# Kernel tuning notes

Measured on AMD Instinct MI355X. Metric: run time of the kernel, lower is better.

Reference implementation:

```python
import jax, jax.numpy as jnp
import numpy as np

D_MODEL = 1024
NUM_HEADS = 16
D_K = D_MODEL // NUM_HEADS
LN_EPS = 1e-5


def setup_inputs() -> dict:
    key = jax.random.key(0)
    ks = jax.random.split(key, 10)
    s = 1.0 / np.sqrt(D_MODEL)
    x = jax.random.normal(ks[0], (4, 2048, D_MODEL), dtype=jnp.float32)
    Wq = jax.random.uniform(ks[1], (D_MODEL, D_MODEL), jnp.float32, -s, s)
    bq = jax.random.uniform(ks[2], (D_MODEL,), jnp.float32, -s, s)
    Wk = jax.random.uniform(ks[3], (D_MODEL, D_MODEL), jnp.float32, -s, s)
    bk = jax.random.uniform(ks[4], (D_MODEL,), jnp.float32, -s, s)
    Wv = jax.random.uniform(ks[5], (D_MODEL, D_MODEL), jnp.float32, -s, s)
    bv = jax.random.uniform(ks[6], (D_MODEL,), jnp.float32, -s, s)
    Wo = jax.random.uniform(ks[7], (D_MODEL, D_MODEL), jnp.float32, -s, s)
    bo = jax.random.uniform(ks[8], (D_MODEL,), jnp.float32, -s, s)
    gamma = jnp.ones((D_MODEL,), jnp.float32)
    beta = jnp.zeros((D_MODEL,), jnp.float32)
    return {"x": x, "Wq": Wq, "bq": bq, "Wk": Wk, "bk": bk, "Wv": Wv,
            "bv": bv, "Wo": Wo, "bo": bo, "gamma": gamma, "beta": beta}


def reference(x, Wq, bq, Wk, bk, Wv, bv, Wo, bo, gamma, beta):
    B, S, D = x.shape
    H, dk = NUM_HEADS, D_K
    # torch Linear: y = x @ W.T + b
    def proj(W, b):
        y = jnp.einsum('bsd,ed->bse', x, W) + b
        return y.reshape(B, S, H, dk).transpose(0, 2, 1, 3)  # [B,H,S,dk]
    Q = proj(Wq, bq)
    K = proj(Wk, bk)
    V = proj(Wv, bv)
    scores = jnp.einsum('bhqd,bhkd->bhqk', Q, K) / np.sqrt(dk)
    attn = jax.nn.softmax(scores, axis=-1)
    head = jnp.einsum('bhqk,bhkd->bhqd', attn, V)
    head = head.transpose(0, 2, 1, 3).reshape(B, S, D)
    out = jnp.einsum('bsd,ed->bse', head, Wo) + bo
    # LayerNorm
    mu = jnp.mean(out, axis=-1, keepdims=True)
    var = jnp.var(out, axis=-1, keepdims=True)
    out = (out - mu) * jax.lax.rsqrt(var + LN_EPS) * gamma + beta
    # dropout is identity in eval mode
    return x + out
```

## Files before the change

### kernel.cpp

```cpp
#include <hip/hip_runtime.h>
#include <stdint.h>

typedef unsigned short u16;
typedef unsigned int u32;
typedef __attribute__((ext_vector_type(8))) short short8;
typedef __attribute__((ext_vector_type(4))) float f32x4;
typedef __attribute__((ext_vector_type(16))) float f32x16;
typedef __attribute__((ext_vector_type(4))) unsigned short u16x4;

#define DEV static __device__ __forceinline__

DEV float bf2f(u16 b) { return __uint_as_float(((uint32_t)b) << 16); }
DEV u16 f2bf(float f) {
  uint32_t u = __float_as_uint(f);
  u += 0x7FFFu + ((u >> 16) & 1u);
  return (u16)(u >> 16);
}
DEV void gld16(const u16* gsrc, u16* ldsdst) {
  __builtin_amdgcn_global_load_lds((const __attribute__((address_space(1))) void*)gsrc,
                                   (__attribute__((address_space(3))) void*)ldsdst, 16, 0, 0);
}
#define MFMA16(a, b, c) __builtin_amdgcn_mfma_f32_16x16x32_bf16(a, b, c, 0, 0, 0)
#define MFMA32(a, b, c) __builtin_amdgcn_mfma_f32_32x32x16_bf16(a, b, c, 0, 0, 0)

#define WAITVM4() asm volatile("s_waitcnt vmcnt(4)" ::: "memory")
#define WAITVM0() asm volatile("s_waitcnt vmcnt(0)" ::: "memory")
DEV void barrier() {
  asm volatile("" ::: "memory");
  __builtin_amdgcn_s_barrier();
  asm volatile("" ::: "memory");
}

#if __has_builtin(__builtin_amdgcn_exp2f)
DEV float fexp2(float x) { return __builtin_amdgcn_exp2f(x); }
#else
DEV float fexp2(float x) { return exp2f(x); }
#endif

DEV u32 cvtpk(float lo, float hi) {
  u32 r;
  asm("v_cvt_pk_bf16_f32 %0, %1, %2" : "=v"(r) : "v"(lo), "v"(hi));
  return r;
}

__global__ __launch_bounds__(256) void k_convert(
    const float* __restrict__ x, const float* __restrict__ wq, const float* __restrict__ wk,
    const float* __restrict__ wv, const float* __restrict__ wo, u16* __restrict__ ws)
{
  int bid = blockIdx.x, t = threadIdx.x;
  const float* src; u16* dst; size_t off;
  if (bid < 8192) { src = x; dst = ws; off = (size_t)bid * 1024; }
  else {
    int r = bid - 8192; int sel = r >> 10; int lb = r & 1023;
    src = sel == 0 ? wq : sel == 1 ? wk : sel == 2 ? wv : wo;
    dst = ws + 8388608u + (size_t)sel * 1048576u;
    off = (size_t)lb * 1024;
  }
  size_t e = off + (size_t)t * 4;
  f32x4 v = *(const f32x4*)(src + e);
  u16x4 o;
  o.x = f2bf(v.x); o.y = f2bf(v.y); o.z = f2bf(v.z); o.w = f2bf(v.w);
  *(u16x4*)(dst + e) = o;
}

DEV void gemm_mainloop(const u16* __restrict__ A, const u16* __restrict__ B,
                       int m0, int n0, u16* As, u16* Bs, f32x4 acc[4][4])
{
  const int tid = threadIdx.x, lane = tid & 63, w = tid >> 6;
  const int fr = lane & 15, g = lane >> 4;
  const int wm = w >> 1, wn = w & 1;

  const int rowA0 = (w * 2 + 0) * 16 + (lane >> 2);
  const int rowA1 = (w * 2 + 1) * 16 + (lane >> 2);
  const int ci = lane & 3;
  const u16* ga0 = A + (size_t)(m0 + rowA0) * 1024 + ((ci ^ (rowA0 & 3)) << 3);
  const u16* ga1 = A + (size_t)(m0 + rowA1) * 1024 + ((ci ^ (rowA1 & 3)) << 3);
  const u16* gb0 = B + (size_t)(n0 + rowA0) * 1024 + ((ci ^ (rowA0 & 3)) << 3);
  const u16* gb1 = B + (size_t)(n0 + rowA1) * 1024 + ((ci ^ (rowA1 & 3)) << 3);
  u16* lA0 = As + (w * 2 + 0) * 512;
  u16* lA1 = As + (w * 2 + 1) * 512;
  u16* lB0 = Bs + (w * 2 + 0) * 512;
  u16* lB1 = Bs + (w * 2 + 1) * 512;

  int raf[4], rbf[4];
#pragma unroll
  for (int i = 0; i < 4; ++i) {
    int rA = wm * 64 + i * 16 + fr;
    raf[i] = rA * 32 + ((g ^ (rA & 3)) << 3);
    int rB = wn * 64 + i * 16 + fr;
    rbf[i] = rB * 32 + ((g ^ (rB & 3)) << 3);
  }

  for (int k0 = 0; k0 < 1024; k0 += 32) {
    __syncthreads();
    gld16(ga0 + k0, lA0);
    gld16(ga1 + k0, lA1);
    gld16(gb0 + k0, lB0);
    gld16(gb1 + k0, lB1);
    __syncthreads();
    short8 af[4], bf[4];
#pragma unroll
    for (int i = 0; i < 4; ++i) af[i] = *(const short8*)&As[raf[i]];
#pragma unroll
    for (int i = 0; i < 4; ++i) bf[i] = *(const short8*)&Bs[rbf[i]];
#pragma unroll
    for (int mi = 0; mi < 4; ++mi)
#pragma unroll
      for (int ni = 0; ni < 4; ++ni)
        acc[mi][ni] = MFMA16(af[mi], bf[ni], acc[mi][ni]);
  }
}

__global__ __launch_bounds__(256) void k_gemm_qkv(
    const u16* __restrict__ xb, const u16* __restrict__ wqb, const u16* __restrict__ wkb,
    const u16* __restrict__ wvb, const float* __restrict__ bq, const float* __restrict__ bk,
    const float* __restrict__ bv, u16* __restrict__ Qg, u16* __restrict__ Kg,
    u16* __restrict__ Vtg)
{
  __shared__ u16 As[128 * 32], Bs[128 * 32];
  const int mb = blockIdx.x, nb_all = blockIdx.y;
  const int mat = nb_all >> 3, nb = nb_all & 7;
  const u16* W = mat == 0 ? wqb : (mat == 1 ? wkb : wvb);
  const float* bias = mat == 0 ? bq : (mat == 1 ? bk : bv);
  const int m0 = mb * 128, n0 = nb * 128;

  f32x4 acc[4][4];
  f32x4 z = {0.f, 0.f, 0.f, 0.f};
#pragma unroll
  for (int i = 0; i < 4; ++i)
#pragma unroll
    for (int j = 0; j < 4; ++j) acc[i][j] = z;

  gemm_mainloop(xb, W, m0, n0, As, Bs, acc);

  const int tid = threadIdx.x, lane = tid & 63, w = tid >> 6;
  const int fr = lane & 15, g = lane >> 4;
  const int wm = w >> 1, wn = w & 1;

  if (mat <= 1) {
    u16* Og = mat == 0 ? Qg : Kg;
    const float scale = mat == 0 ? 0.18033688011112042f : 1.0f;
#pragma unroll
    for (int mi = 0; mi < 4; ++mi)
#pragma unroll
      for (int ni = 0; ni < 4; ++ni) {
        int n = n0 + wn * 64 + ni * 16 + fr;
        float bv_ = bias[n];
        int h = n >> 6, d = n & 63;
#pragma unroll
        for (int r = 0; r < 4; ++r) {
          int m = m0 + wm * 64 + mi * 16 + 4 * g + r;
          int b = m >> 11, s = m & 2047;
          float v = (acc[mi][ni][r] + bv_) * scale;
          Og[(((size_t)(b * 16 + h)) * 2048 + (size_t)s) * 64 + d] = f2bf(v);
        }
      }
  } else {
#pragma unroll
    for (int mi = 0; mi < 4; ++mi)
#pragma unroll
      for (int ni = 0; ni < 4; ++ni) {
        int n = n0 + wn * 64 + ni * 16 + fr;
        float bv_ = bias[n];
        int h = n >> 6, d = n & 63;
        int mbase = m0 + wm * 64 + mi * 16 + 4 * g;
        int b = mbase >> 11, s0 = mbase & 2047;
        u16x4 pk;
        pk.x = f2bf(acc[mi][ni][0] + bv_);
        pk.y = f2bf(acc[mi][ni][1] + bv_);
        pk.z = f2bf(acc[mi][ni][2] + bv_);
        pk.w = f2bf(acc[mi][ni][3] + bv_);
        *(u16x4*)&Vtg[(((size_t)(b * 16 + h)) * 64 + d) * 2048 + s0] = pk;
      }
  }
}

__global__ __launch_bounds__(256) void k_attn(
    const u16* __restrict__ Qg, const u16* __restrict__ Kg, const u16* __restrict__ Vtg,
    u16* __restrict__ headb)
{
  __shared__ u16 K_lds[2][64 * 64];
  __shared__ u16 V_lds[2][64 * 64];
  const int tid = threadIdx.x, lane = tid & 63, w = tid >> 6;
  const int l31 = lane & 31, h5 = lane >> 5, k7 = lane & 7;
  const bool lo_half = (h5 == 0);
  const int swz = ((blockIdx.x & 7) << 7) + (blockIdx.x >> 3);
  const int qb = swz & 15, bh = swz >> 4;
  const u16* Qbase = Qg + (size_t)bh * 2048 * 64;
  const u16* Kbase = Kg + (size_t)bh * 2048 * 64;
  const u16* Vbase = Vtg + (size_t)bh * 64 * 2048;

  const int ck0 = w * 2, ck1 = w * 2 + 1;
  const int srow0 = ck0 * 8 + (lane >> 3), srow1 = ck1 * 8 + (lane >> 3);
  const int sci = lane & 7;
  const u16* gk0 = Kbase + (size_t)srow0 * 64 + ((sci ^ (srow0 & 7)) << 3);
  const u16* gk1 = Kbase + (size_t)srow1 * 64 + ((sci ^ (srow1 & 7)) << 3);
  const u16* gv0 = Vbase + (size_t)srow0 * 2048 + ((sci ^ (srow0 & 7)) << 3);
  const u16* gv1 = Vbase + (size_t)srow1 * 2048 + ((sci ^ (srow1 & 7)) << 3);

  short8 qf[4];
  {
    const u16* qrow = Qbase + (size_t)(qb * 128 + w * 32 + l31) * 64;
#pragma unroll
    for (int j = 0; j < 4; ++j)
      qf[j] = *(const short8*)&qrow[j * 16 + h5 * 8];
  }

  int cj[4];
#pragma unroll
  for (int j = 0; j < 4; ++j) cj[j] = (((2 * j + h5) ^ k7) << 3);
  const int rb = l31 * 64;

  f32x16 po0, po1;
#pragma unroll
  for (int e = 0; e < 16; ++e) { po0[e] = 0.f; po1[e] = 0.f; }
  float mrun = -1e30f, lrun = 0.f;

  gld16(gk0, K_lds[0] + ck0 * 512);
  gld16(gk1, K_lds[0] + ck1 * 512);
  gld16(gv0, V_lds[0] + ck0 * 512);
  gld16(gv1, V_lds[0] + ck1 * 512);

  for (int kv = 0; kv < 32; ++kv) {
    const int cur = kv & 1;
    if (kv < 31) {
      const int ko = (kv + 1) * 64 * 64;
      const int vo = (kv + 1) * 64;
      gld16(gk0 + ko, K_lds[cur ^ 1] + ck0 * 512);
      gld16(gk1 + ko, K_lds[cur ^ 1] + ck1 * 512);
      gld16(gv0 + vo, V_lds[cur ^ 1] + ck0 * 512);
      gld16(gv1 + vo, V_lds[cur ^ 1] + ck1 * 512);
      WAITVM4();
    } else {
      WAITVM0();
    }
    barrier();
    const u16* Kc = K_lds[cur];
    const u16* Vc = V_lds[cur];

    f32x16 s0, s1;
#pragma unroll
    for (int e = 0; e < 16; ++e) { s0[e] = 0.f; s1[e] = 0.f; }
    __builtin_amdgcn_s_setprio(1);
#pragma unroll
    for (int j = 0; j < 4; ++j) {
      short8 kf0 = *(const short8*)&Kc[rb + cj[j]];
      short8 kf1 = *(const short8*)&Kc[2048 + rb + cj[j]];
      s0 = MFMA32(kf0, qf[j], s0);
      s1 = MFMA32(kf1, qf[j], s1);
    }
    __builtin_amdgcn_s_setprio(0);

    float mx = fmaxf(s0[0], s1[0]);
#pragma unroll
    for (int e = 1; e < 16; ++e) mx = fmaxf(mx, fmaxf(s0[e], s1[e]));
    mx = fmaxf(mx, __shfl_xor(mx, 32, 64));
    const bool defer = __all(mx - mrun <= 8.0f);
    const float mnew = defer ? mrun : mx;
#pragma unroll
    for (int e = 0; e < 16; ++e) {
      s0[e] = fexp2(s0[e] - mnew);
      s1[e] = fexp2(s1[e] - mnew);
    }
    float a0 = 0.f, a1 = 0.f, a2 = 0.f, a3 = 0.f;
#pragma unroll
    for (int e = 0; e < 4; ++e) {
      a0 += s0[4 * e + 0] + s1[4 * e + 0];
      a1 += s0[4 * e + 1] + s1[4 * e + 1];
      a2 += s0[4 * e + 2] + s1[4 * e + 2];
      a3 += s0[4 * e + 3] + s1[4 * e + 3];
    }
    float rs = (a0 + a1) + (a2 + a3);
    rs += __shfl_xor(rs, 32, 64);
    if (defer) {
      lrun += rs;
    } else {
      float alpha = fexp2(mrun - mnew);
      lrun = lrun * alpha + rs;
      mrun = mnew;
#pragma unroll
      for (int e = 0; e < 16; ++e) { po0[e] *= alpha; po1[e] *= alpha; }
    }

    __builtin_amdgcn_s_setprio(1);
#pragma unroll
    for (int s = 0; s < 4; ++s) {
      u32 lo0, lo1, hi0, hi1;
      if (s == 0)      { lo0 = cvtpk(s0[0], s0[1]);  lo1 = cvtpk(s0[2], s0[3]);
                         hi0 = cvtpk(s0[4], s0[5]);  hi1 = cvtpk(s0[6], s0[7]); }
      else if (s == 1) { lo0 = cvtpk(s0[8], s0[9]);  lo1 = cvtpk(s0[10], s0[11]);
                         hi0 = cvtpk(s0[12], s0[13]); hi1 = cvtpk(s0[14], s0[15]); }
      else if (s == 2) { lo0 = cvtpk(s1[0], s1[1]);  lo1 = cvtpk(s1[2], s1[3]);
                         hi0 = cvtpk(s1[4], s1[5]);  hi1 = cvtpk(s1[6], s1[7]); }
      else             { lo0 = cvtpk(s1[8], s1[9]);  lo1 = cvtpk(s1[10], s1[11]);
                         hi0 = cvtpk(s1[12], s1[13]); hi1 = cvtpk(s1[14], s1[15]); }
      u32 sent0 = lo_half ? hi0 : lo0;
      u32 sent1 = lo_half ? hi1 : lo1;
      u32 r0 = __shfl_xor(sent0, 32, 64);
      u32 r1 = __shfl_xor(sent1, 32, 64);
      union { u32 u[4]; short8 v; } pf;
      pf.u[0] = lo_half ? lo0 : r0;
      pf.u[1] = lo_half ? lo1 : r1;
      pf.u[2] = lo_half ? r0 : hi0;
      pf.u[3] = lo_half ? r1 : hi1;
      short8 vf0 = *(const short8*)&Vc[rb + cj[s]];
      short8 vf1 = *(const short8*)&Vc[2048 + rb + cj[s]];
      po0 = MFMA32(vf0, pf.v, po0);
      po1 = MFMA32(vf1, pf.v, po1);
    }
    __builtin_amdgcn_s_setprio(0);
    barrier();
  }

  const float linv = 1.0f / lrun;
  const int b = bh >> 4, h = bh & 15;
  const int srow = qb * 128 + w * 32 + l31;
  u16* rowp = headb + (size_t)(b * 2048 + srow) * 1024 + h * 64;
#pragma unroll
  for (int i = 0; i < 4; ++i) {
    u16x4 pk;
    pk.x = f2bf(po0[4 * i + 0] * linv);
    pk.y = f2bf(po0[4 * i + 1] * linv);
    pk.z = f2bf(po0[4 * i + 2] * linv);
    pk.w = f2bf(po0[4 * i + 3] * linv);
    *(u16x4*)&rowp[8 * i + 4 * h5] = pk;
    u16x4 pk2;
    pk2.x = f2bf(po1[4 * i + 0] * linv);
    pk2.y = f2bf(po1[4 * i + 1] * linv);
    pk2.z = f2bf(po1[4 * i + 2] * linv);
    pk2.w = f2bf(po1[4 * i + 3] * linv);
    *(u16x4*)&rowp[32 + 8 * i + 4 * h5] = pk2;
  }
}

__global__ __launch_bounds__(256) void k_gemm_o(
    const u16* __restrict__ headb, const u16* __restrict__ wob, const float* __restrict__ bo,
    u16* __restrict__ projb)
{
  __shared__ u16 As[128 * 32], Bs[128 * 32];
  const int m0 = blockIdx.x * 128, n0 = blockIdx.y * 128;
  f32x4 acc[4][4];
  f32x4 z = {0.f, 0.f, 0.f, 0.f};
#pragma unroll
  for (int i = 0; i < 4; ++i)
#pragma unroll
    for (int j = 0; j < 4; ++j) acc[i][j] = z;

  gemm_mainloop(headb, wob, m0, n0, As, Bs, acc);

  const int tid = threadIdx.x, lane = tid & 63, w = tid >> 6;
  const int fr = lane & 15, g = lane >> 4;
  const int wm = w >> 1, wn = w & 1;
#pragma unroll
  for (int mi = 0; mi < 4; ++mi)
#pragma unroll
    for (int ni = 0; ni < 4; ++ni) {
      int n = n0 + wn * 64 + ni * 16 + fr;
      float bv_ = bo[n];
#pragma unroll
      for (int r = 0; r < 4; ++r) {
        int m = m0 + wm * 64 + mi * 16 + 4 * g + r;
        projb[(size_t)m * 1024 + n] = f2bf(acc[mi][ni][r] + bv_);
      }
    }
}

__global__ __launch_bounds__(256) void k_ln(
    const u16* __restrict__ projb, const float* __restrict__ x,
    const float* __restrict__ gamma, const float* __restrict__ beta, float* __restrict__ out)
{
  __shared__ float sh1[4], sh2[4];
  const int row = blockIdx.x, t = threadIdx.x, lane = t & 63, w = t >> 6;
  const size_t base = (size_t)row * 1024;
  u16x4 pv = *(const u16x4*)&projb[base + t * 4];
  float v0 = bf2f(pv.x), v1 = bf2f(pv.y), v2 = bf2f(pv.z), v3 = bf2f(pv.w);
  float s1 = v0 + v1 + v2 + v3;
  float s2 = v0 * v0 + v1 * v1 + v2 * v2 + v3 * v3;
  for (int m = 1; m < 64; m <<= 1) {
    s1 += __shfl_xor(s1, m, 64);
    s2 += __shfl_xor(s2, m, 64);
  }
  if (lane == 0) { sh1[w] = s1; sh2[w] = s2; }
  __syncthreads();
  s1 = sh1[0] + sh1[1] + sh1[2] + sh1[3];
  s2 = sh2[0] + sh2[1] + sh2[2] + sh2[3];
  float mu = s1 * (1.0f / 1024.0f);
  float var = s2 * (1.0f / 1024.0f) - mu * mu;
  float rsd = rsqrtf(var + 1e-5f);
  f32x4 xv = *(const f32x4*)&x[base + t * 4];
  f32x4 res;
  int e = t * 4;
  res.x = xv.x + (v0 - mu) * rsd * gamma[e + 0] + beta[e + 0];
  res.y = xv.y + (v1 - mu) * rsd * gamma[e + 1] + beta[e + 1];
  res.z = xv.z + (v2 - mu) * rsd * gamma[e + 2] + beta[e + 2];
  res.w = xv.w + (v3 - mu) * rsd * gamma[e + 3] + beta[e + 3];
  *(f32x4*)&out[base + t * 4] = res;
}

extern "C" void kernel_launch(void* const* d_in, const int* in_sizes, int n_in,
                              void* d_out, int out_size, void* d_ws, size_t ws_size,
                              hipStream_t stream)
{
  const float* x     = (const float*)d_in[0];
  const float* Wq    = (const float*)d_in[1];
  const float* bq    = (const float*)d_in[2];
  const float* Wk    = (const float*)d_in[3];
  const float* bk    = (const float*)d_in[4];
  const float* Wv    = (const float*)d_in[5];
  const float* bv    = (const float*)d_in[6];
  const float* Wo    = (const float*)d_in[7];
  const float* bo    = (const float*)d_in[8];
  const float* gamma = (const float*)d_in[9];
  const float* beta  = (const float*)d_in[10];
  float* out = (float*)d_out;

  u16* ws   = (u16*)d_ws;
  u16* xb   = ws;
  u16* wqb  = ws + 8388608;
  u16* wkb  = wqb + 1048576;
  u16* wvb  = wkb + 1048576;
  u16* wob  = wvb + 1048576;
  u16* Qg   = wob + 1048576;
  u16* Kg   = Qg + 8388608;
  u16* Vtg  = Kg + 8388608;
  u16* headb = Vtg + 8388608;
  u16* projb = Qg;

  k_convert<<<12288, 256, 0, stream>>>(x, Wq, Wk, Wv, Wo, ws);
  k_gemm_qkv<<<dim3(64, 24), 256, 0, stream>>>(xb, wqb, wkb, wvb, bq, bk, bv, Qg, Kg, Vtg);
  k_attn<<<dim3(1024), 256, 0, stream>>>(Qg, Kg, Vtg, headb);
  k_gemm_o<<<dim3(64, 8), 256, 0, stream>>>(headb, wob, bo, projb);
  k_ln<<<8192, 256, 0, stream>>>(projb, x, gamma, beta, out);
}
```

Baseline: 241.8 us.

## Give each attention wave private K/V staging to drop block barriers

The attention kernel moves from 4-wave blocks that share 64-key K/V tiles behind two barriers per step to 2-wave blocks of 64 queries. Each wave now loads its own 32-key K/V tiles into private double-buffered LDS, so no block barriers are needed. This removes barrier stalls and lets waves run independently. In exchange, K/V is no longer shared across waves, so global/L2 traffic for K/V roughly quadruples per query and there are twice as many loop iterations with smaller MFMA batches.

```diff
diff --git a/kernel.cpp b/kernel.cpp
--- a/kernel.cpp
+++ b/kernel.cpp
@@ -23,13 +23,8 @@
 #define MFMA16(a, b, c) __builtin_amdgcn_mfma_f32_16x16x32_bf16(a, b, c, 0, 0, 0)
 #define MFMA32(a, b, c) __builtin_amdgcn_mfma_f32_32x32x16_bf16(a, b, c, 0, 0, 0)
 
-#define WAITVM4() asm volatile("s_waitcnt vmcnt(4)" ::: "memory")
+#define WAITVM8() asm volatile("s_waitcnt vmcnt(8)" ::: "memory")
 #define WAITVM0() asm volatile("s_waitcnt vmcnt(0)" ::: "memory")
-DEV void barrier() {
-  asm volatile("" ::: "memory");
-  __builtin_amdgcn_s_barrier();
-  asm volatile("" ::: "memory");
-}
 
 #if __has_builtin(__builtin_amdgcn_exp2f)
 DEV float fexp2(float x) { return __builtin_amdgcn_exp2f(x); }
@@ -175,100 +170,106 @@
   }
 }
 
-__global__ __launch_bounds__(256) void k_attn(
+__global__ __launch_bounds__(128) void k_attn(
     const u16* __restrict__ Qg, const u16* __restrict__ Kg, const u16* __restrict__ Vtg,
     u16* __restrict__ headb)
 {
-  __shared__ u16 K_lds[2][64 * 64];
-  __shared__ u16 V_lds[2][64 * 64];
+  __shared__ u16 KL[2][2][32 * 64];
+  __shared__ u16 VL[2][2][64 * 32];
   const int tid = threadIdx.x, lane = tid & 63, w = tid >> 6;
-  const int l31 = lane & 31, h5 = lane >> 5, k7 = lane & 7;
+  const int l31 = lane & 31, h5 = lane >> 5;
   const bool lo_half = (h5 == 0);
-  const int swz = ((blockIdx.x & 7) << 7) + (blockIdx.x >> 3);
-  const int qb = swz & 15, bh = swz >> 4;
+  const int swz = ((blockIdx.x & 7) << 8) | (blockIdx.x >> 3);
+  const int qb = swz & 31, bh = swz >> 5;
   const u16* Qbase = Qg + (size_t)bh * 2048 * 64;
   const u16* Kbase = Kg + (size_t)bh * 2048 * 64;
   const u16* Vbase = Vtg + (size_t)bh * 64 * 2048;
 
-  const int ck0 = w * 2, ck1 = w * 2 + 1;
-  const int srow0 = ck0 * 8 + (lane >> 3), srow1 = ck1 * 8 + (lane >> 3);
-  const int sci = lane & 7;
-  const u16* gk0 = Kbase + (size_t)srow0 * 64 + ((sci ^ (srow0 & 7)) << 3);
-  const u16* gk1 = Kbase + (size_t)srow1 * 64 + ((sci ^ (srow1 & 7)) << 3);
-  const u16* gv0 = Vbase + (size_t)srow0 * 2048 + ((sci ^ (srow0 & 7)) << 3);
-  const u16* gv1 = Vbase + (size_t)srow1 * 2048 + ((sci ^ (srow1 & 7)) << 3);
+  const int krt = lane >> 3, kci = lane & 7;
+  const int koff = ((kci ^ krt) << 3);
+  const int vrt = lane >> 2, vci = lane & 3;
+  const int voff = ((vci ^ (vrt & 3)) << 3);
+  const u16* gk0 = Kbase + (size_t)(0 * 8 + krt) * 64 + koff;
+  const u16* gk1 = Kbase + (size_t)(1 * 8 + krt) * 64 + koff;
+  const u16* gk2 = Kbase + (size_t)(2 * 8 + krt) * 64 + koff;
+  const u16* gk3 = Kbase + (size_t)(3 * 8 + krt) * 64 + koff;
+  const u16* gv0 = Vbase + (size_t)(0 * 16 + vrt) * 2048 + voff;
+  const u16* gv1 = Vbase + (size_t)(1 * 16 + vrt) * 2048 + voff;
+  const u16* gv2 = Vbase + (size_t)(2 * 16 + vrt) * 2048 + voff;
+  const u16* gv3 = Vbase + (size_t)(3 * 16 + vrt) * 2048 + voff;
 
   short8 qf[4];
   {
-    const u16* qrow = Qbase + (size_t)(qb * 128 + w * 32 + l31) * 64;
+    const u16* qrow = Qbase + (size_t)(qb * 64 + w * 32 + l31) * 64;
 #pragma unroll
     for (int j = 0; j < 4; ++j)
       qf[j] = *(const short8*)&qrow[j * 16 + h5 * 8];
   }
 
-  int cj[4];
-#pragma unroll
-  for (int j = 0; j < 4; ++j) cj[j] = (((2 * j + h5) ^ k7) << 3);
-  const int rb = l31 * 64;
+  int cjK[4], cjV[2];
+#pragma unroll
+  for (int j = 0; j < 4; ++j) cjK[j] = ((2 * j + h5) ^ (l31 & 7)) << 3;
+#pragma unroll
+  for (int s = 0; s < 2; ++s) cjV[s] = ((2 * s + h5) ^ (l31 & 3)) << 3;
 
   f32x16 po0, po1;
 #pragma unroll
   for (int e = 0; e < 16; ++e) { po0[e] = 0.f; po1[e] = 0.f; }
   float mrun = -1e30f, lrun = 0.f;
 
-  gld16(gk0, K_lds[0] + ck0 * 512);
-  gld16(gk1, K_lds[0] + ck1 * 512);
-  gld16(gv0, V_lds[0] + ck0 * 512);
-  gld16(gv1, V_lds[0] + ck1 * 512);
-
-  for (int kv = 0; kv < 32; ++kv) {
+#define STAGE_TILE(kvn, bufsel)                                  \
+  do {                                                           \
+    size_t ko_ = (size_t)(kvn) * 2048;                           \
+    int vo_ = (kvn) * 32;                                        \
+    u16* kd_ = (bufsel) ? KL[w][1] : KL[w][0];                   \
+    u16* vd_ = (bufsel) ? VL[w][1] : VL[w][0];                   \
+    gld16(gk0 + ko_, kd_ + 0 * 512);                             \
+    gld16(gv0 + vo_, vd_ + 0 * 512);                             \
+    gld16(gk1 + ko_, kd_ + 1 * 512);                             \
+    gld16(gv1 + vo_, vd_ + 1 * 512);                             \
+    gld16(gk2 + ko_, kd_ + 2 * 512);                             \
+    gld16(gv2 + vo_, vd_ + 2 * 512);                             \
+    gld16(gk3 + ko_, kd_ + 3 * 512);                             \
+    gld16(gv3 + vo_, vd_ + 3 * 512);                             \
+  } while (0)
+
+  STAGE_TILE(0, 0);
+
+  for (int kv = 0; kv < 64; ++kv) {
     const int cur = kv & 1;
-    if (kv < 31) {
-      const int ko = (kv + 1) * 64 * 64;
-      const int vo = (kv + 1) * 64;
-      gld16(gk0 + ko, K_lds[cur ^ 1] + ck0 * 512);
-      gld16(gk1 + ko, K_lds[cur ^ 1] + ck1 * 512);
-      gld16(gv0 + vo, V_lds[cur ^ 1] + ck0 * 512);
-      gld16(gv1 + vo, V_lds[cur ^ 1] + ck1 * 512);
-      WAITVM4();
+    if (kv < 63) {
+      STAGE_TILE(kv + 1, cur ^ 1);
+      WAITVM8();
     } else {
       WAITVM0();
     }
-    barrier();
-    const u16* Kc = K_lds[cur];
-    const u16* Vc = V_lds[cur];
-
-    f32x16 s0, s1;
-#pragma unroll
-    for (int e = 0; e < 16; ++e) { s0[e] = 0.f; s1[e] = 0.f; }
+    const u16* Kc = cur ? KL[w][1] : KL[w][0];
+    const u16* Vc = cur ? VL[w][1] : VL[w][0];
+
+    f32x16 s0;
+#pragma unroll
+    for (int e = 0; e < 16; ++e) s0[e] = 0.f;
     __builtin_amdgcn_s_setprio(1);
 #pragma unroll
     for (int j = 0; j < 4; ++j) {
-      short8 kf0 = *(const short8*)&Kc[rb + cj[j]];
-      short8 kf1 = *(const short8*)&Kc[2048 + rb + cj[j]];
-      s0 = MFMA32(kf0, qf[j], s0);
-      s1 = MFMA32(kf1, qf[j], s1);
+      short8 kf = *(const short8*)&Kc[l31 * 64 + cjK[j]];
+      s0 = MFMA32(kf, qf[j], s0);
     }
     __builtin_amdgcn_s_setprio(0);
 
-    float mx = fmaxf(s0[0], s1[0]);
-#pragma unroll
-    for (int e = 1; e < 16; ++e) mx = fmaxf(mx, fmaxf(s0[e], s1[e]));
+    float mx = s0[0];
+#pragma unroll
+    for (int e = 1; e < 16; ++e) mx = fmaxf(mx, s0[e]);
     mx = fmaxf(mx, __shfl_xor(mx, 32, 64));
     const bool defer = __all(mx - mrun <= 8.0f);
     const float mnew = defer ? mrun : mx;
 #pragma unroll
-    for (int e = 0; e < 16; ++e) {
-      s0[e] = fexp2(s0[e] - mnew);
-      s1[e] = fexp2(s1[e] - mnew);
-    }
+    for (int e = 0; e < 16; ++e) s0[e] = fexp2(s0[e] - mnew);
     float a0 = 0.f, a1 = 0.f, a2 = 0.f, a3 = 0.f;
 #pragma unroll
     for (int e = 0; e < 4; ++e) {
-      a0 += s0[4 * e + 0] + s1[4 * e + 0];
-      a1 += s0[4 * e + 1] + s1[4 * e + 1];
-      a2 += s0[4 * e + 2] + s1[4 * e + 2];
-      a3 += s0[4 * e + 3] + s1[4 * e + 3];
+      a0 += s0[4 * e + 0]; a1 += s0[4 * e + 1];
+      a2 += s0[4 * e + 2]; a3 += s0[4 * e + 3];
     }
     float rs = (a0 + a1) + (a2 + a3);
     rs += __shfl_xor(rs, 32, 64);
@@ -284,16 +285,11 @@
 
     __builtin_amdgcn_s_setprio(1);
 #pragma unroll
-    for (int s = 0; s < 4; ++s) {
-      u32 lo0, lo1, hi0, hi1;
-      if (s == 0)      { lo0 = cvtpk(s0[0], s0[1]);  lo1 = cvtpk(s0[2], s0[3]);
-                         hi0 = cvtpk(s0[4], s0[5]);  hi1 = cvtpk(s0[6], s0[7]); }
-      else if (s == 1) { lo0 = cvtpk(s0[8], s0[9]);  lo1 = cvtpk(s0[10], s0[11]);
-                         hi0 = cvtpk(s0[12], s0[13]); hi1 = cvtpk(s0[14], s0[15]); }
-      else if (s == 2) { lo0 = cvtpk(s1[0], s1[1]);  lo1 = cvtpk(s1[2], s1[3]);
-                         hi0 = cvtpk(s1[4], s1[5]);  hi1 = cvtpk(s1[6], s1[7]); }
-      else             { lo0 = cvtpk(s1[8], s1[9]);  lo1 = cvtpk(s1[10], s1[11]);
-                         hi0 = cvtpk(s1[12], s1[13]); hi1 = cvtpk(s1[14], s1[15]); }
+    for (int ks = 0; ks < 2; ++ks) {
+      u32 lo0 = cvtpk(s0[8 * ks + 0], s0[8 * ks + 1]);
+      u32 lo1 = cvtpk(s0[8 * ks + 2], s0[8 * ks + 3]);
+      u32 hi0 = cvtpk(s0[8 * ks + 4], s0[8 * ks + 5]);
+      u32 hi1 = cvtpk(s0[8 * ks + 6], s0[8 * ks + 7]);
       u32 sent0 = lo_half ? hi0 : lo0;
       u32 sent1 = lo_half ? hi1 : lo1;
       u32 r0 = __shfl_xor(sent0, 32, 64);
@@ -303,18 +299,18 @@
       pf.u[1] = lo_half ? lo1 : r1;
       pf.u[2] = lo_half ? r0 : hi0;
       pf.u[3] = lo_half ? r1 : hi1;
-      short8 vf0 = *(const short8*)&Vc[rb + cj[s]];
-      short8 vf1 = *(const short8*)&Vc[2048 + rb + cj[s]];
-      po0 = MFMA32(vf0, pf.v, po0);
-      po1 = MFMA32(vf1, pf.v, po1);
+      short8 vfa = *(const short8*)&Vc[l31 * 32 + cjV[ks]];
+      short8 vfb = *(const short8*)&Vc[1024 + l31 * 32 + cjV[ks]];
+      po0 = MFMA32(vfa, pf.v, po0);
+      po1 = MFMA32(vfb, pf.v, po1);
     }
     __builtin_amdgcn_s_setprio(0);
-    barrier();
-  }
+  }
+#undef STAGE_TILE
 
   const float linv = 1.0f / lrun;
   const int b = bh >> 4, h = bh & 15;
-  const int srow = qb * 128 + w * 32 + l31;
+  const int srow = qb * 64 + w * 32 + l31;
   u16* rowp = headb + (size_t)(b * 2048 + srow) * 1024 + h * 64;
 #pragma unroll
   for (int i = 0; i < 4; ++i) {
@@ -428,7 +424,7 @@
 
   k_convert<<<12288, 256, 0, stream>>>(x, Wq, Wk, Wv, Wo, ws);
   k_gemm_qkv<<<dim3(64, 24), 256, 0, stream>>>(xb, wqb, wkb, wvb, bq, bk, bv, Qg, Kg, Vtg);
-  k_attn<<<dim3(1024), 256, 0, stream>>>(Qg, Kg, Vtg, headb);
+  k_attn<<<dim3(2048), 128, 0, stream>>>(Qg, Kg, Vtg, headb);
   k_gemm_o<<<dim3(64, 8), 256, 0, stream>>>(headb, wob, bo, projb);
   k_ln<<<8192, 256, 0, stream>>>(projb, x, gamma, beta, out);
 }
```

New measurement: 294.8 us. 21.9% more time.
